# Performance work log

Hardware: AMD Instinct MI355X
Metric: run time of the kernel (lower is better)

The kernel has to match this reference:

```python
import jax, jax.numpy as jnp
import numpy as np

B, T, D, H = 4, 2048, 1024, 16
HS = D // H

def _layernorm(x, g, b, eps=1e-5):
    mu = jnp.mean(x, axis=-1, keepdims=True)
    var = jnp.var(x, axis=-1, keepdims=True)
    return (x - mu) * jax.lax.rsqrt(var + eps) * g + b

def setup_inputs() -> dict:
    key = jax.random.key(0)
    ks = jax.random.split(key, 8)
    s = 0.02
    return {
        "x": jax.random.normal(ks[0], (B, T, D), jnp.float32),
        "wq": jax.random.normal(ks[1], (D, D), jnp.float32) * s,
        "wk": jax.random.normal(ks[2], (D, D), jnp.float32) * s,
        "wv": jax.random.normal(ks[3], (D, D), jnp.float32) * s,
        "wo": jax.random.normal(ks[4], (D, D), jnp.float32) * s,
        "bo": jnp.zeros((D,), jnp.float32),
        "w1": jax.random.normal(ks[5], (D, 4 * D), jnp.float32) * s,
        "b1": jnp.zeros((4 * D,), jnp.float32),
        "w2": jax.random.normal(ks[6], (4 * D, D), jnp.float32) * s,
        "b2": jnp.zeros((D,), jnp.float32),
        "g1": jnp.ones((D,), jnp.float32),
        "be1": jnp.zeros((D,), jnp.float32),
        "g2": jnp.ones((D,), jnp.float32),
        "be2": jnp.zeros((D,), jnp.float32),
    }

def reference(x, wq, wk, wv, wo, bo, w1, b1, w2, b2, g1, be1, g2, be2):
    b, t, d = x.shape
    h = H
    hs = d // h
    # --- pre-LN + multi-head causal self-attention ---
    xn = _layernorm(x, g1, be1)
    q = (xn @ wq).reshape(b, t, h, hs).transpose(0, 2, 1, 3)  # [b,h,t,hs]
    k = (xn @ wk).reshape(b, t, h, hs).transpose(0, 2, 1, 3)
    v = (xn @ wv).reshape(b, t, h, hs).transpose(0, 2, 1, 3)
    # NOTE: original scales by C**-0.5 where C = embedded_size (not head_size)
    scale = jnp.asarray(d, x.dtype) ** -0.5
    wei = jnp.einsum("bhqd,bhkd->bhqk", q, k) * scale
    causal = jnp.tril(jnp.ones((t, t), bool))
    wei = jnp.where(causal, wei, -jnp.inf)
    wei = jax.nn.softmax(wei, axis=-1)
    attn = jnp.einsum("bhqk,bhkd->bhqd", wei, v)
    attn = attn.transpose(0, 2, 1, 3).reshape(b, t, d)
    x = x + attn @ wo + bo
    # --- pre-LN + FFN ---
    xn2 = _layernorm(x, g2, be2)
    x = x + jax.nn.relu(xn2 @ w1 + b1) @ w2 + b2
    return x
```

## Files before the change

### kernel.cpp

```cpp
#include <hip/hip_runtime.h>
#include <hip/hip_bf16.h>
#include <stdint.h>

typedef __hip_bfloat16 bf16;
typedef __attribute__((ext_vector_type(8))) short bf16x8_t;
typedef __attribute__((ext_vector_type(4))) float f32x4_t;
typedef __attribute__((ext_vector_type(16))) float f32x16_t;
typedef __attribute__((ext_vector_type(2))) unsigned int u32x2_t;

#define B_ 4
#define T_ 2048
#define D_ 1024
#define H_ 16
#define HS_ 64
#define QKV_LD 3072

__device__ __forceinline__ void gload_lds16(const void* g, void* l) {
    __builtin_amdgcn_global_load_lds(
        (const __attribute__((address_space(1))) unsigned int*)g,
        (__attribute__((address_space(3))) unsigned int*)l, 16, 0, 0);
}

__device__ __forceinline__ bf16x8_t ldsv8(const bf16* p) {
    return *(const bf16x8_t*)p;
}

__device__ __forceinline__ unsigned pack2(float a, float b) {
    union { bf16 h[2]; unsigned u; } t;
    t.h[0] = __float2bfloat16(a);
    t.h[1] = __float2bfloat16(b);
    return t.u;
}

__global__ __launch_bounds__(256) void transpose_cvt(
    const float* __restrict__ W, bf16* __restrict__ WT, int K, int N)
{
    __shared__ float tile[32][33];
    const int nbx = N >> 5;
    const int bx = blockIdx.x % nbx;
    const int by = blockIdx.x / nbx;
    const int n0 = bx << 5, k0 = by << 5;
    const int tx = threadIdx.x & 31, ty = threadIdx.x >> 5;
#pragma unroll
    for (int i = 0; i < 32; i += 8)
        tile[ty + i][tx] = W[(long)(k0 + ty + i) * N + n0 + tx];
    __syncthreads();
#pragma unroll
    for (int i = 0; i < 32; i += 8)
        WT[(long)(n0 + ty + i) * K + k0 + tx] = __float2bfloat16(tile[tx][ty + i]);
}

__global__ __launch_bounds__(256) void vhead_transpose(
    const bf16* __restrict__ QKV, bf16* __restrict__ VT)
{
    __shared__ bf16 tile[32][33];
    int idx = blockIdx.x;
    const int tt  = idx & 63;   idx >>= 6;
    const int hst = idx & 1;    idx >>= 1;
    const int bh  = idx;
    const int b = bh >> 4, h = bh & 15;
    const int tx = threadIdx.x & 31, ty = threadIdx.x >> 5;
    const long vrow = (long)b * T_ + tt * 32;
    const int  vcol = 2048 + h * HS_ + hst * 32;
#pragma unroll
    for (int i = 0; i < 32; i += 8)
        tile[ty + i][tx] = QKV[(vrow + ty + i) * QKV_LD + vcol + tx];
    __syncthreads();
    const long orow = (long)bh * HS_ + hst * 32;
#pragma unroll
    for (int i = 0; i < 32; i += 8)
        VT[(orow + ty + i) * T_ + tt * 32 + tx] = tile[tx][ty + i];
}

__global__ __launch_bounds__(256) void ln_k(
    const float* __restrict__ x, const float* __restrict__ g,
    const float* __restrict__ be, bf16* __restrict__ out)
{
    const long row = blockIdx.x;
    const int t = threadIdx.x;
    const float4 v = ((const float4*)(x + row * D_))[t];
    float s  = v.x + v.y + v.z + v.w;
    float s2 = v.x * v.x + v.y * v.y + v.z * v.z + v.w * v.w;
#pragma unroll
    for (int m = 1; m < 64; m <<= 1) {
        s  += __shfl_xor(s, m, 64);
        s2 += __shfl_xor(s2, m, 64);
    }
    __shared__ float red[8];
    const int wv = t >> 6, ln = t & 63;
    if (ln == 0) { red[wv] = s; red[4 + wv] = s2; }
    __syncthreads();
    s  = red[0] + red[1] + red[2] + red[3];
    s2 = red[4] + red[5] + red[6] + red[7];
    const float mu  = s * (1.f / (float)D_);
    const float var = s2 * (1.f / (float)D_) - mu * mu;
    const float rs  = rsqrtf(var + 1e-5f);
    const float4 gv = ((const float4*)g)[t];
    const float4 bv = ((const float4*)be)[t];
    union { bf16 h[4]; short4 s4; } u;
    u.h[0] = __float2bfloat16((v.x - mu) * rs * gv.x + bv.x);
    u.h[1] = __float2bfloat16((v.y - mu) * rs * gv.y + bv.y);
    u.h[2] = __float2bfloat16((v.z - mu) * rs * gv.z + bv.z);
    u.h[3] = __float2bfloat16((v.w - mu) * rs * gv.w + bv.w);
    ((short4*)(out + row * D_))[t] = u.s4;
}

template<int HAS_BIAS, int RELU, int HAS_RES, int OUT_BF16>
__global__ __launch_bounds__(512, 1) void gemm2(
    const bf16* __restrict__ A, const bf16* __restrict__ BT,
    const float* __restrict__ bias, const float* __restrict__ res,
    void* __restrict__ Cout, int M, int N, int K)
{
    __shared__ bf16 As[2][256 * 64];
    __shared__ bf16 Bs[2][128 * 64];
    const int tid  = threadIdx.x;
    const int w    = tid >> 6;
    const int lane = tid & 63;
    const int wm = w >> 1, wn = w & 1;
    const int nbn = N >> 7;
    const int cpx = gridDim.x >> 3;
    const int bid = (blockIdx.x & 7) * cpx + (blockIdx.x >> 3);
    const int bm = bid / nbn, bn = bid % nbn;
    const int row0 = bm << 8, col0 = bn << 7;

    const bf16* aS0; const bf16* aS1; const bf16* aS2; const bf16* aS3;
    const bf16* bS0; const bf16* bS1;
    {
        int f0 = tid,        r0 = f0 >> 3, c0 = ((f0 & 7) ^ (r0 & 7)) << 3;
        int f1 = 512 + tid,  r1 = f1 >> 3, c1 = ((f1 & 7) ^ (r1 & 7)) << 3;
        int f2 = 1024 + tid, r2 = f2 >> 3, c2 = ((f2 & 7) ^ (r2 & 7)) << 3;
        int f3 = 1536 + tid, r3 = f3 >> 3, c3 = ((f3 & 7) ^ (r3 & 7)) << 3;
        aS0 = A + (long)(row0 + r0) * K + c0;
        aS1 = A + (long)(row0 + r1) * K + c1;
        aS2 = A + (long)(row0 + r2) * K + c2;
        aS3 = A + (long)(row0 + r3) * K + c3;
        bS0 = BT + (long)(col0 + r0) * K + c0;
        bS1 = BT + (long)(col0 + r1) * K + c1;
    }
    const int wbase = w * 64;

#define STAGE(buf, kt) do {                                              \
        const long ko_ = (long)(kt) * 64;                                \
        gload_lds16(aS0 + ko_, &As[buf][(0 * 512 + wbase) * 8]);         \
        gload_lds16(aS1 + ko_, &As[buf][(1 * 512 + wbase) * 8]);         \
        gload_lds16(aS2 + ko_, &As[buf][(2 * 512 + wbase) * 8]);         \
        gload_lds16(aS3 + ko_, &As[buf][(3 * 512 + wbase) * 8]);         \
        gload_lds16(bS0 + ko_, &Bs[buf][(0 * 512 + wbase) * 8]);         \
        gload_lds16(bS1 + ko_, &Bs[buf][(1 * 512 + wbase) * 8]);         \
    } while (0)

    f32x4_t acc[4][4] = {};
    const int fr = lane & 15;
    const int fq = lane >> 4;
    const int nt = K >> 6;

    STAGE(0, 0);
    STAGE(1, 1);

    for (int t = 0; t < nt; ++t) {
        const int cur = t & 1;
        if (t < nt - 1) asm volatile("s_waitcnt vmcnt(6)" ::: "memory");
        else            asm volatile("s_waitcnt vmcnt(0)" ::: "memory");
        __builtin_amdgcn_s_barrier();

        bf16x8_t a[2][4], b[2][4];
#pragma unroll
        for (int ks = 0; ks < 2; ++ks) {
#pragma unroll
            for (int m = 0; m < 4; ++m) {
                const int r = wm * 64 + m * 16 + fr;
                const int ch = ks * 4 + fq;
                a[ks][m] = ldsv8(&As[cur][r * 64 + ((ch ^ (r & 7)) << 3)]);
            }
#pragma unroll
            for (int n = 0; n < 4; ++n) {
                const int r = wn * 64 + n * 16 + fr;
                const int ch = ks * 4 + fq;
                b[ks][n] = ldsv8(&Bs[cur][r * 64 + ((ch ^ (r & 7)) << 3)]);
            }
        }
        asm volatile("s_waitcnt lgkmcnt(0)" ::: "memory");
        __builtin_amdgcn_sched_barrier(0);
        __builtin_amdgcn_s_barrier();

        if (t + 2 < nt) STAGE(cur, t + 2);

        __builtin_amdgcn_s_setprio(1);
#pragma unroll
        for (int m = 0; m < 4; ++m)
#pragma unroll
            for (int n = 0; n < 4; ++n) {
                acc[m][n] = __builtin_amdgcn_mfma_f32_16x16x32_bf16(a[0][m], b[0][n], acc[m][n], 0, 0, 0);
                acc[m][n] = __builtin_amdgcn_mfma_f32_16x16x32_bf16(a[1][m], b[1][n], acc[m][n], 0, 0, 0);
            }
        __builtin_amdgcn_s_setprio(0);
    }
#undef STAGE

    const int orow = fq << 2;
#pragma unroll
    for (int m = 0; m < 4; ++m) {
        const int rbase = row0 + wm * 64 + m * 16 + orow;
#pragma unroll
        for (int n = 0; n < 4; ++n) {
            const int c = col0 + wn * 64 + n * 16 + fr;
            float bv = 0.f;
            if (HAS_BIAS) bv = bias[c];
#pragma unroll
            for (int r = 0; r < 4; ++r) {
                float v = acc[m][n][r] + bv;
                if (RELU) v = fmaxf(v, 0.f);
                if (HAS_RES) v += res[(long)(rbase + r) * N + c];
                if (OUT_BF16)
                    ((bf16*)Cout)[(long)(rbase + r) * N + c] = __float2bfloat16(v);
                else
                    ((float*)Cout)[(long)(rbase + r) * N + c] = v;
            }
        }
    }
}

__global__ __launch_bounds__(512, 2) void attn_flash(
    const bf16* __restrict__ QKV, const bf16* __restrict__ VT,
    bf16* __restrict__ O)
{
    __shared__ bf16 Ks[2][64 * 64];
    __shared__ bf16 Vs[2][64 * 64];

    const int tid = threadIdx.x;
    const int w   = tid >> 6;
    const int ln  = tid & 63;
    const int l31 = ln & 31;
    const int hi  = ln >> 5;
    const int hi8 = hi << 3;

    const int qb = 7 - (int)blockIdx.x;
    const int bh = blockIdx.y;
    const long rowBase = (long)(bh >> 4) * T_;
    const int colBase = (bh & 15) * HS_;

    const int qwbase = qb * 256 + w * 32;
    const int qabs   = qwbase + l31;
    const int ctb  = qb * 4 + 3;
    const int ct_w = qb * 4 + (w >> 1);

    const bf16* qp = QKV + (rowBase + qabs) * QKV_LD + colBase + hi8;
    bf16x8_t qf[4];
#pragma unroll
    for (int s = 0; s < 4; ++s) qf[s] = *(const bf16x8_t*)(qp + 16 * s);

    f32x16_t oA = {}, oB = {};
    float mOld = -1e30f, lSum = 0.f;
    const float kE  = 0.0450842200278f;
    const float THR = 256.0f;

    const int srow = tid >> 3;
    const int schunk = (((tid & 7) ^ (srow & 7)) << 3);
    const bf16* kSrc = QKV + (rowBase + srow) * QKV_LD + 1024 + colBase + schunk;
    const bf16* vSrc = VT + ((long)bh * HS_ + srow) * T_ + schunk;

    gload_lds16(kSrc, &Ks[0][w * 512]);
    gload_lds16(vSrc, &Vs[0][w * 512]);

    const int swzk = (l31 & 7) << 3;

    for (int c = 0; c <= ctb; ++c) {
        const int cur = c & 1;
        __syncthreads();

        if (c < ctb) {
            gload_lds16(kSrc + (long)(c + 1) * 64 * QKV_LD, &Ks[cur ^ 1][w * 512]);
            gload_lds16(vSrc + (c + 1) * 64, &Vs[cur ^ 1][w * 512]);
        }
        if (c > ct_w) continue;

        const bf16* K_ = Ks[cur];
        const bf16* V_ = Vs[cur];
        const bool diag = (c == ct_w);
        const bool two  = !(diag && !(w & 1));

        f32x16_t s0 = {}, s1 = {};
#pragma unroll
        for (int s = 0; s < 4; ++s) {
            bf16x8_t kf = ldsv8(K_ + l31 * 64 + ((16 * s + hi8) ^ swzk));
            s0 = __builtin_amdgcn_mfma_f32_32x32x16_bf16(kf, qf[s], s0, 0, 0, 0);
        }
        if (two) {
#pragma unroll
            for (int s = 0; s < 4; ++s) {
                bf16x8_t kf = ldsv8(K_ + (32 + l31) * 64 + ((16 * s + hi8) ^ swzk));
                s1 = __builtin_amdgcn_mfma_f32_32x32x16_bf16(kf, qf[s], s1, 0, 0, 0);
            }
        }

        if (diag) {
            const int stm = w & 1;
            const int kb0 = c * 64 + stm * 32 + 4 * hi;
            if (stm) {
#pragma unroll
                for (int r = 0; r < 16; ++r)
                    if (kb0 + (r & 3) + 8 * (r >> 2) > qabs) s1[r] = -1e30f;
            } else {
#pragma unroll
                for (int r = 0; r < 16; ++r)
                    if (kb0 + (r & 3) + 8 * (r >> 2) > qabs) s0[r] = -1e30f;
            }
        }

        float rm = s0[0];
#pragma unroll
        for (int r = 1; r < 16; ++r) rm = fmaxf(rm, s0[r]);
        if (two) {
#pragma unroll
            for (int r = 0; r < 16; ++r) rm = fmaxf(rm, s1[r]);
        }
        {
            u32x2_t rr = __builtin_amdgcn_permlane32_swap(
                __float_as_uint(rm), __float_as_uint(rm), false, false);
            rm = fmaxf(__uint_as_float(rr.x), __uint_as_float(rr.y));
        }
        if (!__all(rm <= mOld + THR)) {
            const float mN = fmaxf(mOld, rm);
            const float corr = exp2f((mOld - mN) * kE);
#pragma unroll
            for (int r = 0; r < 16; ++r) { oA[r] *= corr; oB[r] *= corr; }
            lSum *= corr;
            mOld = mN;
        }
        const float nmk = -mOld * kE;
#pragma unroll
        for (int r = 0; r < 16; ++r) s0[r] = exp2f(fmaf(s0[r], kE, nmk));
        if (two) {
#pragma unroll
            for (int r = 0; r < 16; ++r) s1[r] = exp2f(fmaf(s1[r], kE, nmk));
        }
        float rs = s0[0];
#pragma unroll
        for (int r = 1; r < 16; ++r) rs += s0[r];
        if (two) {
#pragma unroll
            for (int r = 0; r < 16; ++r) rs += s1[r];
        }
        {
            u32x2_t rr = __builtin_amdgcn_permlane32_swap(
                __float_as_uint(rs), __float_as_uint(rs), false, false);
            rs = __uint_as_float(rr.x) + __uint_as_float(rr.y);
        }
        lSum += rs;

        {
            unsigned pk_[8];
#pragma unroll
            for (int i = 0; i < 8; ++i) pk_[i] = pack2(s0[2 * i], s0[2 * i + 1]);
            union { unsigned u[4]; bf16x8_t v; } W0, W1;
            u32x2_t ra = __builtin_amdgcn_permlane32_swap(pk_[0], pk_[2], false, false);
            u32x2_t rb = __builtin_amdgcn_permlane32_swap(pk_[1], pk_[3], false, false);
            W0.u[0] = ra.x; W0.u[1] = rb.x; W0.u[2] = ra.y; W0.u[3] = rb.y;
            u32x2_t rc = __builtin_amdgcn_permlane32_swap(pk_[4], pk_[6], false, false);
            u32x2_t rd = __builtin_amdgcn_permlane32_swap(pk_[5], pk_[7], false, false);
            W1.u[0] = rc.x; W1.u[1] = rd.x; W1.u[2] = rc.y; W1.u[3] = rd.y;
#pragma unroll
            for (int m = 0; m < 2; ++m) {
                const int kcol = 16 * m + hi8;
                bf16x8_t vf0 = ldsv8(V_ + l31 * 64 + (kcol ^ swzk));
                oA = __builtin_amdgcn_mfma_f32_32x32x16_bf16(vf0, m ? W1.v : W0.v, oA, 0, 0, 0);
                bf16x8_t vf1 = ldsv8(V_ + (32 + l31) * 64 + (kcol ^ swzk));
                oB = __builtin_amdgcn_mfma_f32_32x32x16_bf16(vf1, m ? W1.v : W0.v, oB, 0, 0, 0);
            }
        }
        if (two) {
            unsigned pk_[8];
#pragma unroll
            for (int i = 0; i < 8; ++i) pk_[i] = pack2(s1[2 * i], s1[2 * i + 1]);
            union { unsigned u[4]; bf16x8_t v; } W0, W1;
            u32x2_t ra = __builtin_amdgcn_permlane32_swap(pk_[0], pk_[2], false, false);
            u32x2_t rb = __builtin_amdgcn_permlane32_swap(pk_[1], pk_[3], false, false);
            W0.u[0] = ra.x; W0.u[1] = rb.x; W0.u[2] = ra.y; W0.u[3] = rb.y;
            u32x2_t rc = __builtin_amdgcn_permlane32_swap(pk_[4], pk_[6], false, false);
            u32x2_t rd = __builtin_amdgcn_permlane32_swap(pk_[5], pk_[7], false, false);
            W1.u[0] = rc.x; W1.u[1] = rd.x; W1.u[2] = rc.y; W1.u[3] = rd.y;
#pragma unroll
            for (int m = 0; m < 2; ++m) {
                const int kcol = 16 * (2 + m) + hi8;
                bf16x8_t vf0 = ldsv8(V_ + l31 * 64 + (kcol ^ swzk));
                oA = __builtin_amdgcn_mfma_f32_32x32x16_bf16(vf0, m ? W1.v : W0.v, oA, 0, 0, 0);
                bf16x8_t vf1 = ldsv8(V_ + (32 + l31) * 64 + (kcol ^ swzk));
                oB = __builtin_amdgcn_mfma_f32_32x32x16_bf16(vf1, m ? W1.v : W0.v, oB, 0, 0, 0);
            }
        }
    }

    const float inv = 1.f / lSum;
    bf16* Op = O + (rowBase + qabs) * D_ + colBase;
#pragma unroll
    for (int g = 0; g < 4; ++g) {
        u32x2_t sA, sB;
        sA.x = pack2(oA[4 * g + 0] * inv, oA[4 * g + 1] * inv);
        sA.y = pack2(oA[4 * g + 2] * inv, oA[4 * g + 3] * inv);
        sB.x = pack2(oB[4 * g + 0] * inv, oB[4 * g + 1] * inv);
        sB.y = pack2(oB[4 * g + 2] * inv, oB[4 * g + 3] * inv);
        *(u32x2_t*)(Op + 8 * g + 4 * hi)      = sA;
        *(u32x2_t*)(Op + 32 + 8 * g + 4 * hi) = sB;
    }
}

extern "C" void kernel_launch(void* const* d_in, const int* in_sizes, int n_in,
                              void* d_out, int out_size, void* d_ws, size_t ws_size,
                              hipStream_t stream)
{
    (void)in_sizes; (void)n_in; (void)out_size; (void)ws_size;
    const float* x   = (const float*)d_in[0];
    const float* wq  = (const float*)d_in[1];
    const float* wk  = (const float*)d_in[2];
    const float* wv  = (const float*)d_in[3];
    const float* wo  = (const float*)d_in[4];
    const float* bo  = (const float*)d_in[5];
    const float* w1  = (const float*)d_in[6];
    const float* b1  = (const float*)d_in[7];
    const float* w2  = (const float*)d_in[8];
    const float* b2  = (const float*)d_in[9];
    const float* g1  = (const float*)d_in[10];
    const float* be1 = (const float*)d_in[11];
    const float* g2  = (const float*)d_in[12];
    const float* be2 = (const float*)d_in[13];
    float* out = (float*)d_out;

    char* ws = (char*)d_ws;
    const size_t SLOT = (size_t)8192 * 1024 * 2;
    bf16* xn     = (bf16*)(ws);
    bf16* attnb  = (bf16*)(ws);
    bf16* qkv    = (bf16*)(ws + SLOT);
    bf16* xn2    = (bf16*)(ws + SLOT);
    bf16* vtb    = (bf16*)(ws + 4 * SLOT);
    bf16* hidden = (bf16*)(ws + 2 * SLOT);
    float* x1    = (float*)(ws + 6 * SLOT);
    char* wpos   = ws + 6 * SLOT + (size_t)33554432;
    bf16* wqkvT = (bf16*)(wpos);
    bf16* wqT = (bf16*)(wpos);
    bf16* wkT = (bf16*)(wpos + (size_t)2097152);
    bf16* wvT = (bf16*)(wpos + (size_t)2 * 2097152);
    bf16* woT = (bf16*)(wpos + (size_t)3 * 2097152);
    bf16* w1T = (bf16*)(wpos + (size_t)4 * 2097152);
    bf16* w2T = (bf16*)(wpos + (size_t)4 * 2097152 + 8388608);

    transpose_cvt<<<dim3(1024), 256, 0, stream>>>(wq, wqT, 1024, 1024);
    transpose_cvt<<<dim3(1024), 256, 0, stream>>>(wk, wkT, 1024, 1024);
    transpose_cvt<<<dim3(1024), 256, 0, stream>>>(wv, wvT, 1024, 1024);
    transpose_cvt<<<dim3(1024), 256, 0, stream>>>(wo, woT, 1024, 1024);
    transpose_cvt<<<dim3(4096), 256, 0, stream>>>(w1, w1T, 1024, 4096);
    transpose_cvt<<<dim3(4096), 256, 0, stream>>>(w2, w2T, 4096, 1024);

    ln_k<<<8192, 256, 0, stream>>>(x, g1, be1, xn);

    gemm2<0, 0, 0, 1><<<768, 512, 0, stream>>>(xn, wqkvT, nullptr, nullptr, qkv, 8192, 3072, 1024);

    vhead_transpose<<<8192, 256, 0, stream>>>(qkv, vtb);

    attn_flash<<<dim3(8, 64), 512, 0, stream>>>(qkv, vtb, attnb);

    gemm2<1, 0, 1, 0><<<256, 512, 0, stream>>>(attnb, woT, bo, x, x1, 8192, 1024, 1024);

    ln_k<<<8192, 256, 0, stream>>>(x1, g2, be2, xn2);

    gemm2<1, 1, 0, 1><<<1024, 512, 0, stream>>>(xn2, w1T, b1, nullptr, hidden, 8192, 4096, 1024);

    gemm2<1, 0, 1, 0><<<256, 512, 0, stream>>>(hidden, w2T, b2, x1, out, 8192, 1024, 4096);
}
```

Before: 535.8 us.

## Pair low and high causal query blocks per workgroup to share K/V tiles

Each attention workgroup now handles two query blocks, a low one (qLo) and its mirror high one (7-qLo). This balances causal work across workgroups and lets the low block reuse the K/V tiles already staged in LDS for the high block. The grid is halved to 4x64 and launch bounds drop to one block per CU to make room for twice the accumulator registers. The cost is lower occupancy and only 256 workgroups, which may leave CUs underused.

```diff
diff --git a/kernel.cpp b/kernel.cpp
--- a/kernel.cpp
+++ b/kernel.cpp
@@ -220,7 +220,128 @@
     }
 }
 
-__global__ __launch_bounds__(512, 2) void attn_flash(
+__device__ __forceinline__ void attn_tile(
+    const bf16* K_, const bf16* V_, const bf16x8_t (&qf)[4],
+    f32x16_t& oA, f32x16_t& oB, float& mOld, float& lSum,
+    int c, int ct_w, int qabs, int w, int l31, int hi, int hi8, int swzk)
+{
+    const float kE  = 0.0450842200278f;
+    const float THR = 256.0f;
+    const bool diag = (c == ct_w);
+    const bool two  = !(diag && !(w & 1));
+
+    f32x16_t s0 = {}, s1 = {};
+#pragma unroll
+    for (int s = 0; s < 4; ++s) {
+        bf16x8_t kf = ldsv8(K_ + l31 * 64 + ((16 * s + hi8) ^ swzk));
+        s0 = __builtin_amdgcn_mfma_f32_32x32x16_bf16(kf, qf[s], s0, 0, 0, 0);
+    }
+    if (two) {
+#pragma unroll
+        for (int s = 0; s < 4; ++s) {
+            bf16x8_t kf = ldsv8(K_ + (32 + l31) * 64 + ((16 * s + hi8) ^ swzk));
+            s1 = __builtin_amdgcn_mfma_f32_32x32x16_bf16(kf, qf[s], s1, 0, 0, 0);
+        }
+    }
+
+    if (diag) {
+        const int stm = w & 1;
+        const int kb0 = c * 64 + stm * 32 + 4 * hi;
+        if (stm) {
+#pragma unroll
+            for (int r = 0; r < 16; ++r)
+                if (kb0 + (r & 3) + 8 * (r >> 2) > qabs) s1[r] = -1e30f;
+        } else {
+#pragma unroll
+            for (int r = 0; r < 16; ++r)
+                if (kb0 + (r & 3) + 8 * (r >> 2) > qabs) s0[r] = -1e30f;
+        }
+    }
+
+    float rm = s0[0];
+#pragma unroll
+    for (int r = 1; r < 16; ++r) rm = fmaxf(rm, s0[r]);
+    if (two) {
+#pragma unroll
+        for (int r = 0; r < 16; ++r) rm = fmaxf(rm, s1[r]);
+    }
+    {
+        u32x2_t rr = __builtin_amdgcn_permlane32_swap(
+            __float_as_uint(rm), __float_as_uint(rm), false, false);
+        rm = fmaxf(__uint_as_float(rr.x), __uint_as_float(rr.y));
+    }
+    if (!__all(rm <= mOld + THR)) {
+        const float mN = fmaxf(mOld, rm);
+        const float corr = exp2f((mOld - mN) * kE);
+#pragma unroll
+        for (int r = 0; r < 16; ++r) { oA[r] *= corr; oB[r] *= corr; }
+        lSum *= corr;
+        mOld = mN;
+    }
+    const float nmk = -mOld * kE;
+#pragma unroll
+    for (int r = 0; r < 16; ++r) s0[r] = exp2f(fmaf(s0[r], kE, nmk));
+    if (two) {
+#pragma unroll
+        for (int r = 0; r < 16; ++r) s1[r] = exp2f(fmaf(s1[r], kE, nmk));
+    }
+    float rs = s0[0];
+#pragma unroll
+    for (int r = 1; r < 16; ++r) rs += s0[r];
+    if (two) {
+#pragma unroll
+        for (int r = 0; r < 16; ++r) rs += s1[r];
+    }
+    {
+        u32x2_t rr = __builtin_amdgcn_permlane32_swap(
+            __float_as_uint(rs), __float_as_uint(rs), false, false);
+        rs = __uint_as_float(rr.x) + __uint_as_float(rr.y);
+    }
+    lSum += rs;
+
+    {
+        unsigned pk_[8];
+#pragma unroll
+        for (int i = 0; i < 8; ++i) pk_[i] = pack2(s0[2 * i], s0[2 * i + 1]);
+        union { unsigned u[4]; bf16x8_t v; } W0, W1;
+        u32x2_t ra = __builtin_amdgcn_permlane32_swap(pk_[0], pk_[2], false, false);
+        u32x2_t rb = __builtin_amdgcn_permlane32_swap(pk_[1], pk_[3], false, false);
+        W0.u[0] = ra.x; W0.u[1] = rb.x; W0.u[2] = ra.y; W0.u[3] = rb.y;
+        u32x2_t rc = __builtin_amdgcn_permlane32_swap(pk_[4], pk_[6], false, false);
+        u32x2_t rd = __builtin_amdgcn_permlane32_swap(pk_[5], pk_[7], false, false);
+        W1.u[0] = rc.x; W1.u[1] = rd.x; W1.u[2] = rc.y; W1.u[3] = rd.y;
+#pragma unroll
+        for (int m = 0; m < 2; ++m) {
+            const int kcol = 16 * m + hi8;
+            bf16x8_t vf0 = ldsv8(V_ + l31 * 64 + (kcol ^ swzk));
+            oA = __builtin_amdgcn_mfma_f32_32x32x16_bf16(vf0, m ? W1.v : W0.v, oA, 0, 0, 0);
+            bf16x8_t vf1 = ldsv8(V_ + (32 + l31) * 64 + (kcol ^ swzk));
+            oB = __builtin_amdgcn_mfma_f32_32x32x16_bf16(vf1, m ? W1.v : W0.v, oB, 0, 0, 0);
+        }
+    }
+    if (two) {
+        unsigned pk_[8];
+#pragma unroll
+        for (int i = 0; i < 8; ++i) pk_[i] = pack2(s1[2 * i], s1[2 * i + 1]);
+        union { unsigned u[4]; bf16x8_t v; } W0, W1;
+        u32x2_t ra = __builtin_amdgcn_permlane32_swap(pk_[0], pk_[2], false, false);
+        u32x2_t rb = __builtin_amdgcn_permlane32_swap(pk_[1], pk_[3], false, false);
+        W0.u[0] = ra.x; W0.u[1] = rb.x; W0.u[2] = ra.y; W0.u[3] = rb.y;
+        u32x2_t rc = __builtin_amdgcn_permlane32_swap(pk_[4], pk_[6], false, false);
+        u32x2_t rd = __builtin_amdgcn_permlane32_swap(pk_[5], pk_[7], false, false);
+        W1.u[0] = rc.x; W1.u[1] = rd.x; W1.u[2] = rc.y; W1.u[3] = rd.y;
+#pragma unroll
+        for (int m = 0; m < 2; ++m) {
+            const int kcol = 16 * (2 + m) + hi8;
+            bf16x8_t vf0 = ldsv8(V_ + l31 * 64 + (kcol ^ swzk));
+            oA = __builtin_amdgcn_mfma_f32_32x32x16_bf16(vf0, m ? W1.v : W0.v, oA, 0, 0, 0);
+            bf16x8_t vf1 = ldsv8(V_ + (32 + l31) * 64 + (kcol ^ swzk));
+            oB = __builtin_amdgcn_mfma_f32_32x32x16_bf16(vf1, m ? W1.v : W0.v, oB, 0, 0, 0);
+        }
+    }
+}
+
+__global__ __launch_bounds__(512, 1) void attn_flash(
     const bf16* __restrict__ QKV, const bf16* __restrict__ VT,
     bf16* __restrict__ O)
 {
@@ -234,25 +355,31 @@
     const int hi  = ln >> 5;
     const int hi8 = hi << 3;
 
-    const int qb = 7 - (int)blockIdx.x;
+    const int qLo = blockIdx.x;
+    const int qHi = 7 - qLo;
     const int bh = blockIdx.y;
     const long rowBase = (long)(bh >> 4) * T_;
     const int colBase = (bh & 15) * HS_;
 
-    const int qwbase = qb * 256 + w * 32;
-    const int qabs   = qwbase + l31;
-    const int ctb  = qb * 4 + 3;
-    const int ct_w = qb * 4 + (w >> 1);
-
-    const bf16* qp = QKV + (rowBase + qabs) * QKV_LD + colBase + hi8;
-    bf16x8_t qf[4];
-#pragma unroll
-    for (int s = 0; s < 4; ++s) qf[s] = *(const bf16x8_t*)(qp + 16 * s);
-
-    f32x16_t oA = {}, oB = {};
-    float mOld = -1e30f, lSum = 0.f;
-    const float kE  = 0.0450842200278f;
-    const float THR = 256.0f;
+    const int qabsL = qLo * 256 + w * 32 + l31;
+    const int qabsH = qHi * 256 + w * 32 + l31;
+    const int ct_L  = qLo * 4 + (w >> 1);
+    const int ct_H  = qHi * 4 + (w >> 1);
+    const int ctb   = qHi * 4 + 3;
+
+    bf16x8_t qfL[4], qfH[4];
+    {
+        const bf16* qpL = QKV + (rowBase + qabsL) * QKV_LD + colBase + hi8;
+        const bf16* qpH = QKV + (rowBase + qabsH) * QKV_LD + colBase + hi8;
+#pragma unroll
+        for (int s = 0; s < 4; ++s) {
+            qfL[s] = *(const bf16x8_t*)(qpL + 16 * s);
+            qfH[s] = *(const bf16x8_t*)(qpH + 16 * s);
+        }
+    }
+
+    f32x16_t oLA = {}, oLB = {}, oHA = {}, oHB = {};
+    float mL = -1e30f, lL = 0.f, mH = -1e30f, lH = 0.f;
 
     const int srow = tid >> 3;
     const int schunk = (((tid & 7) ^ (srow & 7)) << 3);
@@ -272,135 +399,42 @@
             gload_lds16(kSrc + (long)(c + 1) * 64 * QKV_LD, &Ks[cur ^ 1][w * 512]);
             gload_lds16(vSrc + (c + 1) * 64, &Vs[cur ^ 1][w * 512]);
         }
-        if (c > ct_w) continue;
 
         const bf16* K_ = Ks[cur];
         const bf16* V_ = Vs[cur];
-        const bool diag = (c == ct_w);
-        const bool two  = !(diag && !(w & 1));
-
-        f32x16_t s0 = {}, s1 = {};
-#pragma unroll
-        for (int s = 0; s < 4; ++s) {
-            bf16x8_t kf = ldsv8(K_ + l31 * 64 + ((16 * s + hi8) ^ swzk));
-            s0 = __builtin_amdgcn_mfma_f32_32x32x16_bf16(kf, qf[s], s0, 0, 0, 0);
-        }
-        if (two) {
-#pragma unroll
-            for (int s = 0; s < 4; ++s) {
-                bf16x8_t kf = ldsv8(K_ + (32 + l31) * 64 + ((16 * s + hi8) ^ swzk));
-                s1 = __builtin_amdgcn_mfma_f32_32x32x16_bf16(kf, qf[s], s1, 0, 0, 0);
-            }
-        }
-
-        if (diag) {
-            const int stm = w & 1;
-            const int kb0 = c * 64 + stm * 32 + 4 * hi;
-            if (stm) {
-#pragma unroll
-                for (int r = 0; r < 16; ++r)
-                    if (kb0 + (r & 3) + 8 * (r >> 2) > qabs) s1[r] = -1e30f;
-            } else {
-#pragma unroll
-                for (int r = 0; r < 16; ++r)
-                    if (kb0 + (r & 3) + 8 * (r >> 2) > qabs) s0[r] = -1e30f;
-            }
-        }
-
-        float rm = s0[0];
-#pragma unroll
-        for (int r = 1; r < 16; ++r) rm = fmaxf(rm, s0[r]);
-        if (two) {
-#pragma unroll
-            for (int r = 0; r < 16; ++r) rm = fmaxf(rm, s1[r]);
-        }
-        {
-            u32x2_t rr = __builtin_amdgcn_permlane32_swap(
-                __float_as_uint(rm), __float_as_uint(rm), false, false);
-            rm = fmaxf(__uint_as_float(rr.x), __uint_as_float(rr.y));
-        }
-        if (!__all(rm <= mOld + THR)) {
-            const float mN = fmaxf(mOld, rm);
-            const float corr = exp2f((mOld - mN) * kE);
-#pragma unroll
-            for (int r = 0; r < 16; ++r) { oA[r] *= corr; oB[r] *= corr; }
-            lSum *= corr;
-            mOld = mN;
-        }
-        const float nmk = -mOld * kE;
-#pragma unroll
-        for (int r = 0; r < 16; ++r) s0[r] = exp2f(fmaf(s0[r], kE, nmk));
-        if (two) {
-#pragma unroll
-            for (int r = 0; r < 16; ++r) s1[r] = exp2f(fmaf(s1[r], kE, nmk));
-        }
-        float rs = s0[0];
-#pragma unroll
-        for (int r = 1; r < 16; ++r) rs += s0[r];
-        if (two) {
-#pragma unroll
-            for (int r = 0; r < 16; ++r) rs += s1[r];
-        }
-        {
-            u32x2_t rr = __builtin_amdgcn_permlane32_swap(
-                __float_as_uint(rs), __float_as_uint(rs), false, false);
-            rs = __uint_as_float(rr.x) + __uint_as_float(rr.y);
-        }
-        lSum += rs;
-
-        {
-            unsigned pk_[8];
-#pragma unroll
-            for (int i = 0; i < 8; ++i) pk_[i] = pack2(s0[2 * i], s0[2 * i + 1]);
-            union { unsigned u[4]; bf16x8_t v; } W0, W1;
-            u32x2_t ra = __builtin_amdgcn_permlane32_swap(pk_[0], pk_[2], false, false);
-            u32x2_t rb = __builtin_amdgcn_permlane32_swap(pk_[1], pk_[3], false, false);
-            W0.u[0] = ra.x; W0.u[1] = rb.x; W0.u[2] = ra.y; W0.u[3] = rb.y;
-            u32x2_t rc = __builtin_amdgcn_permlane32_swap(pk_[4], pk_[6], false, false);
-            u32x2_t rd = __builtin_amdgcn_permlane32_swap(pk_[5], pk_[7], false, false);
-            W1.u[0] = rc.x; W1.u[1] = rd.x; W1.u[2] = rc.y; W1.u[3] = rd.y;
-#pragma unroll
-            for (int m = 0; m < 2; ++m) {
-                const int kcol = 16 * m + hi8;
-                bf16x8_t vf0 = ldsv8(V_ + l31 * 64 + (kcol ^ swzk));
-                oA = __builtin_amdgcn_mfma_f32_32x32x16_bf16(vf0, m ? W1.v : W0.v, oA, 0, 0, 0);
-                bf16x8_t vf1 = ldsv8(V_ + (32 + l31) * 64 + (kcol ^ swzk));
-                oB = __builtin_amdgcn_mfma_f32_32x32x16_bf16(vf1, m ? W1.v : W0.v, oB, 0, 0, 0);
-            }
-        }
-        if (two) {
-            unsigned pk_[8];
-#pragma unroll
-            for (int i = 0; i < 8; ++i) pk_[i] = pack2(s1[2 * i], s1[2 * i + 1]);
-            union { unsigned u[4]; bf16x8_t v; } W0, W1;
-            u32x2_t ra = __builtin_amdgcn_permlane32_swap(pk_[0], pk_[2], false, false);
-            u32x2_t rb = __builtin_amdgcn_permlane32_swap(pk_[1], pk_[3], false, false);
-            W0.u[0] = ra.x; W0.u[1] = rb.x; W0.u[2] = ra.y; W0.u[3] = rb.y;
-            u32x2_t rc = __builtin_amdgcn_permlane32_swap(pk_[4], pk_[6], false, false);
-            u32x2_t rd = __builtin_amdgcn_permlane32_swap(pk_[5], pk_[7], false, false);
-            W1.u[0] = rc.x; W1.u[1] = rd.x; W1.u[2] = rc.y; W1.u[3] = rd.y;
-#pragma unroll
-            for (int m = 0; m < 2; ++m) {
-                const int kcol = 16 * (2 + m) + hi8;
-                bf16x8_t vf0 = ldsv8(V_ + l31 * 64 + (kcol ^ swzk));
-                oA = __builtin_amdgcn_mfma_f32_32x32x16_bf16(vf0, m ? W1.v : W0.v, oA, 0, 0, 0);
-                bf16x8_t vf1 = ldsv8(V_ + (32 + l31) * 64 + (kcol ^ swzk));
-                oB = __builtin_amdgcn_mfma_f32_32x32x16_bf16(vf1, m ? W1.v : W0.v, oB, 0, 0, 0);
-            }
-        }
-    }
-
-    const float inv = 1.f / lSum;
-    bf16* Op = O + (rowBase + qabs) * D_ + colBase;
-#pragma unroll
-    for (int g = 0; g < 4; ++g) {
-        u32x2_t sA, sB;
-        sA.x = pack2(oA[4 * g + 0] * inv, oA[4 * g + 1] * inv);
-        sA.y = pack2(oA[4 * g + 2] * inv, oA[4 * g + 3] * inv);
-        sB.x = pack2(oB[4 * g + 0] * inv, oB[4 * g + 1] * inv);
-        sB.y = pack2(oB[4 * g + 2] * inv, oB[4 * g + 3] * inv);
-        *(u32x2_t*)(Op + 8 * g + 4 * hi)      = sA;
-        *(u32x2_t*)(Op + 32 + 8 * g + 4 * hi) = sB;
+        if (c <= ct_H)
+            attn_tile(K_, V_, qfH, oHA, oHB, mH, lH, c, ct_H, qabsH, w, l31, hi, hi8, swzk);
+        if (c <= ct_L)
+            attn_tile(K_, V_, qfL, oLA, oLB, mL, lL, c, ct_L, qabsL, w, l31, hi, hi8, swzk);
+    }
+
+    {
+        const float inv = 1.f / lH;
+        bf16* Op = O + (rowBase + qabsH) * D_ + colBase;
+#pragma unroll
+        for (int g = 0; g < 4; ++g) {
+            u32x2_t sA, sB;
+            sA.x = pack2(oHA[4 * g + 0] * inv, oHA[4 * g + 1] * inv);
+            sA.y = pack2(oHA[4 * g + 2] * inv, oHA[4 * g + 3] * inv);
+            sB.x = pack2(oHB[4 * g + 0] * inv, oHB[4 * g + 1] * inv);
+            sB.y = pack2(oHB[4 * g + 2] * inv, oHB[4 * g + 3] * inv);
+            *(u32x2_t*)(Op + 8 * g + 4 * hi)      = sA;
+            *(u32x2_t*)(Op + 32 + 8 * g + 4 * hi) = sB;
+        }
+    }
+    {
+        const float inv = 1.f / lL;
+        bf16* Op = O + (rowBase + qabsL) * D_ + colBase;
+#pragma unroll
+        for (int g = 0; g < 4; ++g) {
+            u32x2_t sA, sB;
+            sA.x = pack2(oLA[4 * g + 0] * inv, oLA[4 * g + 1] * inv);
+            sA.y = pack2(oLA[4 * g + 2] * inv, oLA[4 * g + 3] * inv);
+            sB.x = pack2(oLB[4 * g + 0] * inv, oLB[4 * g + 1] * inv);
+            sB.y = pack2(oLB[4 * g + 2] * inv, oLB[4 * g + 3] * inv);
+            *(u32x2_t*)(Op + 8 * g + 4 * hi)      = sA;
+            *(u32x2_t*)(Op + 32 + 8 * g + 4 * hi) = sB;
+        }
     }
 }
 
@@ -456,7 +490,7 @@
 
     vhead_transpose<<<8192, 256, 0, stream>>>(qkv, vtb);
 
-    attn_flash<<<dim3(8, 64), 512, 0, stream>>>(qkv, vtb, attnb);
+    attn_flash<<<dim3(4, 64), 512, 0, stream>>>(qkv, vtb, attnb);
 
     gemm2<1, 0, 1, 0><<<256, 512, 0, stream>>>(attnb, woT, bo, x, x1, 8192, 1024, 1024);
 
```

New measurement: 504.3 us. -5.9%, faster.
